# Optimization experiments

Measured on AMD Instinct MI355X. Metric: run time of the kernel, lower is better.

The kernel has to match this reference:

```python
import jax, jax.numpy as jnp
import numpy as np

NUM_HEADS = 16
HEAD_SIZE = 64
D_MODEL = NUM_HEADS * HEAD_SIZE  # 1024


def setup_inputs() -> dict:
    key = jax.random.key(0)
    ks = jax.random.split(key, 12)
    B, S = 4, 2048
    q = jax.random.normal(ks[0], (B, S, D_MODEL), dtype=jnp.float32)
    k = jax.random.normal(ks[1], (B, S, D_MODEL), dtype=jnp.float32)
    v = jax.random.normal(ks[2], (B, S, D_MODEL), dtype=jnp.float32)
    w = jax.random.uniform(ks[3], (B, S), dtype=jnp.float32)
    scale = 1.0 / np.sqrt(D_MODEL)
    Wq = jax.random.normal(ks[4], (D_MODEL, D_MODEL), dtype=jnp.float32) * scale
    Wk = jax.random.normal(ks[5], (D_MODEL, D_MODEL), dtype=jnp.float32) * scale
    Wv = jax.random.normal(ks[6], (D_MODEL, D_MODEL), dtype=jnp.float32) * scale
    Wo = jax.random.normal(ks[7], (D_MODEL, D_MODEL), dtype=jnp.float32) * scale
    bq = jnp.zeros((D_MODEL,), jnp.float32)
    bk = jnp.zeros((D_MODEL,), jnp.float32)
    bv = jnp.zeros((D_MODEL,), jnp.float32)
    bo = jnp.zeros((D_MODEL,), jnp.float32)
    return {"q": q, "k": k, "v": v, "w": w,
            "Wq": Wq, "bq": bq, "Wk": Wk, "bk": bk,
            "Wv": Wv, "bv": bv, "Wo": Wo, "bo": bo}


def reference(q, k, v, w, Wq, bq, Wk, bk, Wv, bv, Wo, bo):
    B, S, _ = q.shape
    H, Dh = NUM_HEADS, HEAD_SIZE

    def split_heads(x):  # [B,S,D] -> [B,H,S,Dh]
        return x.reshape(B, -1, H, Dh).transpose(0, 2, 1, 3)

    q_h = split_heads(q @ Wq + bq)
    k_h = split_heads(k @ Wk + bk)
    v_h = split_heads(v @ Wv + bv)

    # [B,H,Sq,Sk]
    score = jnp.einsum('bhqd,bhkd->bhqk', q_h, k_h) / jnp.sqrt(
        jnp.asarray(Dh, jnp.float32))
    # weighted unnormalized softmax: exp(score)*w / sum (no max subtraction,
    # faithful to original)
    exp_score = jnp.exp(score) * w[:, None, None, :]
    attn = exp_score / (jnp.sum(exp_score, axis=-1, keepdims=True) + 1e-12)

    context = jnp.einsum('bhqk,bhkd->bhqd', attn, v_h)  # [B,H,S,Dh]
    context = context.transpose(0, 2, 1, 3).reshape(B, -1, H * Dh)
    return context @ Wo + bo
```

## Files before the change

### kernel.cpp

```cpp
#include <hip/hip_runtime.h>
#include <hip/hip_bf16.h>

typedef __bf16 bf16x8 __attribute__((ext_vector_type(8)));
typedef float f32x4 __attribute__((ext_vector_type(4)));
typedef float f32x16 __attribute__((ext_vector_type(16)));
typedef unsigned short u16;
typedef unsigned int u32;

#define SB 4
#define SS 2048
#define SD 1024
#define SH 16
#define SDH 64

__device__ __forceinline__ u16 f2bf(float f) {
  union { float f; u32 u; } x; x.f = f;
  u32 r = (x.u + 0x7FFFu + ((x.u >> 16) & 1u)) >> 16;
  return (u16)r;
}

__device__ __forceinline__ void gl_lds16(const void* g, void* l) {
  __builtin_amdgcn_global_load_lds(
      (__attribute__((address_space(1))) void*)g,
      (__attribute__((address_space(3))) void*)l, 16, 0, 0);
}

__global__ void cast_bf16_kernel(const float* __restrict__ in,
                                 u32* __restrict__ out, int n8) {
  int i = blockIdx.x * blockDim.x + threadIdx.x;
  if (i >= n8) return;
  const float4* inp = (const float4*)in;
  float4 a = inp[2 * i], b = inp[2 * i + 1];
  uint4 o;
  asm("v_cvt_pk_bf16_f32 %0, %1, %2" : "=v"(o.x) : "v"(a.x), "v"(a.y));
  asm("v_cvt_pk_bf16_f32 %0, %1, %2" : "=v"(o.y) : "v"(a.z), "v"(a.w));
  asm("v_cvt_pk_bf16_f32 %0, %1, %2" : "=v"(o.z) : "v"(b.x), "v"(b.y));
  asm("v_cvt_pk_bf16_f32 %0, %1, %2" : "=v"(o.w) : "v"(b.z), "v"(b.w));
  ((uint4*)out)[i] = o;
}

__global__ void log2w_kernel(const float* __restrict__ w,
                             float* __restrict__ lwg) {
  int i = blockIdx.x * 256 + threadIdx.x;
  lwg[i] = __builtin_amdgcn_logf(w[i]);
}

__global__ void transpose_cast_kernel(const float* __restrict__ W0,
                                      const float* __restrict__ W1,
                                      const float* __restrict__ W2,
                                      const float* __restrict__ W3,
                                      u16* __restrict__ T0,
                                      u16* __restrict__ T1,
                                      u16* __restrict__ T2,
                                      u16* __restrict__ T3) {
  __shared__ float t[32][33];
  int z = blockIdx.z;
  const float* W = (z == 0) ? W0 : (z == 1) ? W1 : (z == 2) ? W2 : W3;
  u16* Wt = (z == 0) ? T0 : (z == 1) ? T1 : (z == 2) ? T2 : T3;
  int bx = blockIdx.x, by = blockIdx.y;
  int tx = threadIdx.x, ty = threadIdx.y;
#pragma unroll
  for (int j = 0; j < 32; j += 8)
    t[ty + j][tx] = W[(size_t)(by * 32 + ty + j) * SD + bx * 32 + tx];
  __syncthreads();
#pragma unroll
  for (int j = 0; j < 32; j += 8)
    Wt[(size_t)(bx * 32 + ty + j) * SD + by * 32 + tx] = f2bf(t[tx][ty + j]);
}

template <int MODE>
__global__ __launch_bounds__(256, 2)
void gemm_bt(const u16* __restrict__ A, const u16* __restrict__ Bt,
             const float* __restrict__ bias, void* __restrict__ Out,
             int M, int N, int K) {
  __shared__ u16 Asl[2][128 * 64];
  __shared__ u16 Bsl[2][128 * 64];
  const int ntile = N >> 7;
  int bid = blockIdx.x;
  bid = (bid & 7) * ((int)gridDim.x >> 3) + (bid >> 3);
  int m0 = (bid / ntile) * 128, n0 = (bid % ntile) * 128;
  int tid = threadIdx.x;
  int lane = tid & 63, wv = tid >> 6;
  int wr = wv >> 1, wc = wv & 1;

  auto stage = [&](int buf, int k0) {
#pragma unroll
    for (int it = 0; it < 4; ++it) {
      int c = tid + it * 256;
      int row = c >> 3, sl = c & 7;
      int ssl = sl ^ (row & 7);
      gl_lds16(A + (size_t)(m0 + row) * K + k0 + ssl * 8,
               (char*)&Asl[buf][0] + c * 16);
      gl_lds16(Bt + (size_t)(n0 + row) * K + k0 + ssl * 8,
               (char*)&Bsl[buf][0] + c * 16);
    }
  };

  f32x4 acc[4][4] = {};
  stage(0, 0);

  int nk = K >> 6;
  for (int kt = 0; kt < nk; ++kt) {
    int buf = kt & 1;
    if (kt + 1 < nk) {
      stage(buf ^ 1, (kt + 1) << 6);
      asm volatile("s_waitcnt vmcnt(8) lgkmcnt(0)" ::: "memory");
    } else {
      asm volatile("s_waitcnt vmcnt(0) lgkmcnt(0)" ::: "memory");
    }
    __builtin_amdgcn_s_barrier();
#pragma unroll
    for (int kk = 0; kk < 2; ++kk) {
      bf16x8 af[4], bfr[4];
#pragma unroll
      for (int i = 0; i < 4; ++i) {
        int ar = wr * 64 + i * 16 + (lane & 15);
        int abyt = (ar * 128 + (kk * 32 + (lane >> 4) * 8) * 2) ^
                   ((ar & 7) << 4);
        af[i] = *(const bf16x8*)((const char*)&Asl[buf][0] + abyt);
        int br = wc * 64 + i * 16 + (lane & 15);
        int bbyt = (br * 128 + (kk * 32 + (lane >> 4) * 8) * 2) ^
                   ((br & 7) << 4);
        bfr[i] = *(const bf16x8*)((const char*)&Bsl[buf][0] + bbyt);
      }
#pragma unroll
      for (int i = 0; i < 4; ++i)
#pragma unroll
        for (int j = 0; j < 4; ++j)
          acc[i][j] = __builtin_amdgcn_mfma_f32_16x16x32_bf16(
              af[i], bfr[j], acc[i][j], 0, 0, 0);
    }
    __builtin_amdgcn_s_barrier();
  }

  int cg = lane >> 4, cc = lane & 15;
#pragma unroll
  for (int i = 0; i < 4; ++i) {
#pragma unroll
    for (int j = 0; j < 4; ++j) {
#pragma unroll
      for (int r = 0; r < 4; ++r) {
        int m = m0 + wr * 64 + i * 16 + cg * 4 + r;
        int n = n0 + wc * 64 + j * 16 + cc;
        float val = acc[i][j][r];
        if (MODE == 0) {
          val = (val + bias[n]) * 0.18033688011112042f;
          int b = m >> 11, s = m & 2047, h = n >> 6, dh = n & 63;
          ((u16*)Out)[((size_t)((b * SH + h) * SS + s) << 6) + dh] = f2bf(val);
        } else if (MODE == 1) {
          val += bias[n];
          int b = m >> 11, s = m & 2047, h = n >> 6, dh = n & 63;
          size_t off = ((size_t)(b * SH + h) << 17) + ((size_t)(s >> 5) << 11) +
                       ((size_t)(dh >> 4) << 9) +
                       ((size_t)((s & 31) | ((dh & 8) << 2)) << 3) + (dh & 7);
          ((u16*)Out)[off] = f2bf(val);
        } else if (MODE == 2) {
          val += bias[m];
          int h = m >> 6, dh = m & 63, b = n >> 11, s = n & 2047;
          size_t off = ((size_t)(b * SH + h) << 17) + ((size_t)(s >> 4) << 10) +
                       ((size_t)(dh >> 5) << 9) +
                       ((size_t)(((s >> 3) & 1) * 32 + (dh & 31)) << 3) +
                       (s & 7);
          ((u16*)Out)[off] = f2bf(val);
        } else {
          val += bias[n];
          ((float*)Out)[(size_t)m * N + n] = val;
        }
      }
    }
  }
}

__global__ __launch_bounds__(256, 2)
void attn_kernel(const u16* __restrict__ Qh, const u16* __restrict__ Kf,
                 const u16* __restrict__ Vf, const float* __restrict__ lwg,
                 u16* __restrict__ Ctx) {
  __shared__ u16 Kl[4][4096];
  __shared__ u16 Vl[4][4096];

  int bid = blockIdx.x;
  int swz = (bid & 7) * 64 + (bid >> 3);
  int bh = swz >> 3;
  int qt = swz & 7;
  int b = bh >> 4, hh = bh & 15;
  int q0 = qt * 256;
  int tid = threadIdx.x, lane = tid & 63, wv = tid >> 6;
  int ql = lane & 31, h = lane >> 5;
  const size_t basebh = (size_t)bh * (SS * SDH);
  const char* Ksrc = (const char*)(Kf + basebh);
  const char* Vsrc = (const char*)(Vf + basebh);
  const float* lwp = lwg + b * SS;

  bf16x8 qf[2][4];
#pragma unroll
  for (int u = 0; u < 2; ++u) {
    const u16* qp =
        Qh + basebh + (size_t)(q0 + wv * 64 + u * 32 + ql) * SDH + h * 8;
#pragma unroll
    for (int st = 0; st < 4; ++st) qf[u][st] = *(const bf16x8*)(qp + st * 16);
  }

  auto stage = [&](int s, int t) {
#pragma unroll
    for (int it = 0; it < 2; ++it) {
      int c = tid + it * 256;
      gl_lds16(Ksrc + (size_t)t * 8192 + c * 16, (char*)&Kl[s][0] + c * 16);
      gl_lds16(Vsrc + (size_t)t * 8192 + c * 16, (char*)&Vl[s][0] + c * 16);
    }
  };

  f32x16 ctx[2][2] = {};
  float rs[2] = {0.f, 0.f};
  u32 pkA[2][8][2], pkB[2][8][2];

  auto qk = [&](int t, u32 (&pk)[2][8][2]) {
    const char* Ks = (const char*)&Kl[t & 3][0];
    int kvb = t * 64;
#pragma unroll
    for (int kt = 0; kt < 2; ++kt) {
      bf16x8 kf[4];
#pragma unroll
      for (int st = 0; st < 4; ++st)
        kf[st] = *(const bf16x8*)(Ks + (kt * 4 + st) * 1024 + lane * 16);
      float4 lw[4];
#pragma unroll
      for (int e2 = 0; e2 < 4; ++e2)
        lw[e2] = *(const float4*)(lwp + kvb + kt * 32 + e2 * 8 + h * 4);
#pragma unroll
      for (int u = 0; u < 2; ++u) {
        f32x16 sc;
#pragma unroll
        for (int e2 = 0; e2 < 4; ++e2) {
          sc[e2 * 4 + 0] = lw[e2].x;
          sc[e2 * 4 + 1] = lw[e2].y;
          sc[e2 * 4 + 2] = lw[e2].z;
          sc[e2 * 4 + 3] = lw[e2].w;
        }
        __builtin_amdgcn_s_setprio(1);
#pragma unroll
        for (int st = 0; st < 4; ++st)
          sc = __builtin_amdgcn_mfma_f32_32x32x16_bf16(kf[st], qf[u][st], sc,
                                                       0, 0, 0);
        __builtin_amdgcn_s_setprio(0);
#pragma unroll
        for (int e2 = 0; e2 < 4; ++e2) {
          float v0 = __builtin_amdgcn_exp2f(sc[e2 * 4 + 0]);
          float v1 = __builtin_amdgcn_exp2f(sc[e2 * 4 + 1]);
          float v2 = __builtin_amdgcn_exp2f(sc[e2 * 4 + 2]);
          float v3 = __builtin_amdgcn_exp2f(sc[e2 * 4 + 3]);
          rs[u] += (v0 + v1) + (v2 + v3);
          u32 p0, p1;
          asm("v_cvt_pk_bf16_f32 %0, %1, %2" : "=v"(p0) : "v"(v0), "v"(v1));
          asm("v_cvt_pk_bf16_f32 %0, %1, %2" : "=v"(p1) : "v"(v2), "v"(v3));
          pk[u][kt * 4 + e2][0] = p0;
          pk[u][kt * 4 + e2][1] = p1;
        }
      }
    }
  };

  auto pv = [&](int t, u32 (&pk)[2][8][2]) {
    const char* Vs = (const char*)&Vl[t & 3][0];
#pragma unroll
    for (int ksl = 0; ksl < 4; ++ksl) {
      bf16x8 vf0 = *(const bf16x8*)(Vs + (ksl * 2 + 0) * 1024 + lane * 16);
      bf16x8 vf1 = *(const bf16x8*)(Vs + (ksl * 2 + 1) * 1024 + lane * 16);
#pragma unroll
      for (int u = 0; u < 2; ++u) {
        u32 d0 = pk[u][2 * ksl][0], d1 = pk[u][2 * ksl][1];
        u32 s0 = pk[u][2 * ksl + 1][0], s1 = pk[u][2 * ksl + 1][1];
        asm("v_permlane32_swap_b32 %0, %1" : "+v"(d0), "+v"(s0));
        asm("v_permlane32_swap_b32 %0, %1" : "+v"(d1), "+v"(s1));
        union { u32 uu[4]; bf16x8 v; } pa;
        pa.uu[0] = d0; pa.uu[1] = d1; pa.uu[2] = s0; pa.uu[3] = s1;
        __builtin_amdgcn_s_setprio(1);
        ctx[u][0] = __builtin_amdgcn_mfma_f32_32x32x16_bf16(pa.v, vf0,
                                                            ctx[u][0], 0, 0, 0);
        ctx[u][1] = __builtin_amdgcn_mfma_f32_32x32x16_bf16(pa.v, vf1,
                                                            ctx[u][1], 0, 0, 0);
        __builtin_amdgcn_s_setprio(0);
      }
    }
  };

  stage(0, 0);
  stage(1, 1);

  asm volatile("s_waitcnt vmcnt(4)" ::: "memory");
  __builtin_amdgcn_s_barrier();
  stage(2, 2);
  qk(0, pkA);

  for (int t = 1; t < 30; t += 2) {
    asm volatile("s_waitcnt vmcnt(4)" ::: "memory");
    __builtin_amdgcn_s_barrier();
    stage((t + 2) & 3, t + 2);
    pv(t - 1, pkA);
    qk(t, pkB);

    asm volatile("s_waitcnt vmcnt(4)" ::: "memory");
    __builtin_amdgcn_s_barrier();
    if (t + 3 < 32) stage((t + 3) & 3, t + 3);
    pv(t, pkB);
    qk(t + 1, pkA);
  }

  asm volatile("s_waitcnt vmcnt(0)" ::: "memory");
  __builtin_amdgcn_s_barrier();
  pv(30, pkA);
  qk(31, pkB);
  pv(31, pkB);

#pragma unroll
  for (int u = 0; u < 2; ++u) {
    float rsu = rs[u];
    rsu += __shfl_xor(rsu, 32, 64);
    float rinv = 1.0f / (rsu + 1e-12f);
#pragma unroll
    for (int reg = 0; reg < 16; ++reg) {
      int qrow = (reg & 3) + 8 * (reg >> 2) + 4 * h;
      float ri = __shfl(rinv, qrow, 64);
      int srow = q0 + wv * 64 + u * 32 + qrow;
      size_t base = ((size_t)(b * SS + srow) << 10) + hh * SDH;
      Ctx[base + ql] = f2bf(ctx[u][0][reg] * ri);
      Ctx[base + 32 + ql] = f2bf(ctx[u][1][reg] * ri);
    }
  }
}

extern "C" void kernel_launch(void* const* d_in, const int* in_sizes, int n_in,
                              void* d_out, int out_size, void* d_ws,
                              size_t ws_size, hipStream_t stream) {
  const float* q = (const float*)d_in[0];
  const float* k = (const float*)d_in[1];
  const float* v = (const float*)d_in[2];
  const float* w = (const float*)d_in[3];
  const float* Wq = (const float*)d_in[4];
  const float* bq = (const float*)d_in[5];
  const float* Wk = (const float*)d_in[6];
  const float* bk = (const float*)d_in[7];
  const float* Wv = (const float*)d_in[8];
  const float* bv = (const float*)d_in[9];
  const float* Wo = (const float*)d_in[10];
  const float* bo = (const float*)d_in[11];
  float* out = (float*)d_out;

  char* ws = (char*)d_ws;
  const size_t SZ = (size_t)8192 * 1024 * 2;
  u16* qb = (u16*)(ws);
  u16* kb = (u16*)(ws + SZ);
  u16* vb = (u16*)(ws + 2 * SZ);
  u16* WqT = (u16*)(ws + 3 * SZ);
  u16* WkT = WqT + 1024 * 1024;
  u16* WvT = WkT + 1024 * 1024;
  u16* WoT = WvT + 1024 * 1024;
  u16* Qh = (u16*)(ws + 3 * SZ + (size_t)4 * 1024 * 1024 * 2);
  u16* Kf = Qh + (size_t)8192 * 1024;
  u16* Vf = Kf + (size_t)8192 * 1024;
  float* lwg = (float*)(ws + 3 * SZ + (size_t)4 * 1024 * 1024 * 2 +
                        (size_t)3 * 8192 * 1024 * 2);
  u16* Ctx = qb;

  cast_bf16_kernel<<<4096, 256, 0, stream>>>(q, (u32*)qb, 1048576);
  cast_bf16_kernel<<<4096, 256, 0, stream>>>(k, (u32*)kb, 1048576);
  cast_bf16_kernel<<<4096, 256, 0, stream>>>(v, (u32*)vb, 1048576);
  log2w_kernel<<<32, 256, 0, stream>>>(w, lwg);
  dim3 tb(32, 8), tg(32, 32, 4);
  transpose_cast_kernel<<<tg, tb, 0, stream>>>(Wq, Wk, Wv, Wo,
                                               WqT, WkT, WvT, WoT);

  gemm_bt<0><<<512, 256, 0, stream>>>(qb, WqT, bq, Qh, 8192, 1024, 1024);
  gemm_bt<1><<<512, 256, 0, stream>>>(kb, WkT, bk, Kf, 8192, 1024, 1024);
  gemm_bt<2><<<512, 256, 0, stream>>>(WvT, vb, bv, Vf, 1024, 8192, 1024);

  attn_kernel<<<512, 256, 0, stream>>>(Qh, Kf, Vf, lwg, Ctx);

  gemm_bt<3><<<512, 256, 0, stream>>>(Ctx, WoT, bo, out, 8192, 1024, 1024);
}
```

Baseline: 210.2 us.

## Split attention KV sequence across two wave groups with LDS reduction

The attention block grows to 512 threads. Each of the two halves of 4 waves processes half the KV tiles (a split-K over keys) using its own double-buffered LDS region, and the partial context and row sums are then reduced through shared memory before normalization and store. The QK and PV phases are merged into one per-tile compute step, and the pipeline changes from a 4-stage software-pipelined ping-pong to a simpler 2-stage wait-all loop. The aim is more waves per CU to hide latency, at the cost of a less overlapped pipeline, 64KB of LDS per block, and extra reduction barriers.

```diff
diff --git a/kernel.cpp b/kernel.cpp
--- a/kernel.cpp
+++ b/kernel.cpp
@@ -3,6 +3,7 @@
 
 typedef __bf16 bf16x8 __attribute__((ext_vector_type(8)));
 typedef float f32x4 __attribute__((ext_vector_type(4)));
+typedef float f32x8 __attribute__((ext_vector_type(8)));
 typedef float f32x16 __attribute__((ext_vector_type(16)));
 typedef unsigned short u16;
 typedef unsigned int u32;
@@ -171,12 +172,11 @@
   }
 }
 
-__global__ __launch_bounds__(256, 2)
+__global__ __launch_bounds__(512, 4)
 void attn_kernel(const u16* __restrict__ Qh, const u16* __restrict__ Kf,
                  const u16* __restrict__ Vf, const float* __restrict__ lwg,
                  u16* __restrict__ Ctx) {
-  __shared__ u16 Kl[4][4096];
-  __shared__ u16 Vl[4][4096];
+  __shared__ __align__(16) char smem[65536];
 
   int bid = blockIdx.x;
   int swz = (bid & 7) * 64 + (bid >> 3);
@@ -185,60 +185,65 @@
   int b = bh >> 4, hh = bh & 15;
   int q0 = qt * 256;
   int tid = threadIdx.x, lane = tid & 63, wv = tid >> 6;
+  int qw = wv & 3, kvh = wv >> 2;
   int ql = lane & 31, h = lane >> 5;
+  int tl = tid & 255;
   const size_t basebh = (size_t)bh * (SS * SDH);
   const char* Ksrc = (const char*)(Kf + basebh);
   const char* Vsrc = (const char*)(Vf + basebh);
   const float* lwp = lwg + b * SS;
+  char* mybase = smem + kvh * 32768;
 
   bf16x8 qf[2][4];
 #pragma unroll
   for (int u = 0; u < 2; ++u) {
     const u16* qp =
-        Qh + basebh + (size_t)(q0 + wv * 64 + u * 32 + ql) * SDH + h * 8;
+        Qh + basebh + (size_t)(q0 + qw * 64 + u * 32 + ql) * SDH + h * 8;
 #pragma unroll
     for (int st = 0; st < 4; ++st) qf[u][st] = *(const bf16x8*)(qp + st * 16);
   }
 
-  auto stage = [&](int s, int t) {
+  auto stage = [&](int s, int th) {
+    char* dst = mybase + s * 16384;
 #pragma unroll
     for (int it = 0; it < 2; ++it) {
-      int c = tid + it * 256;
-      gl_lds16(Ksrc + (size_t)t * 8192 + c * 16, (char*)&Kl[s][0] + c * 16);
-      gl_lds16(Vsrc + (size_t)t * 8192 + c * 16, (char*)&Vl[s][0] + c * 16);
+      int c = tl + it * 256;
+      gl_lds16(Ksrc + (size_t)th * 8192 + c * 16, dst + c * 16);
+      gl_lds16(Vsrc + (size_t)th * 8192 + c * 16, dst + 8192 + c * 16);
     }
   };
 
   f32x16 ctx[2][2] = {};
   float rs[2] = {0.f, 0.f};
-  u32 pkA[2][8][2], pkB[2][8][2];
-
-  auto qk = [&](int t, u32 (&pk)[2][8][2]) {
-    const char* Ks = (const char*)&Kl[t & 3][0];
-    int kvb = t * 64;
+
+  auto compute = [&](int s, int th) {
+    const char* Ks = mybase + s * 16384;
+    const char* Vs = Ks + 8192;
+    int kvb = th * 64;
+    u32 pk[2][8][2];
 #pragma unroll
     for (int kt = 0; kt < 2; ++kt) {
       bf16x8 kf[4];
 #pragma unroll
       for (int st = 0; st < 4; ++st)
         kf[st] = *(const bf16x8*)(Ks + (kt * 4 + st) * 1024 + lane * 16);
-      float4 lw[4];
-#pragma unroll
-      for (int e2 = 0; e2 < 4; ++e2)
-        lw[e2] = *(const float4*)(lwp + kvb + kt * 32 + e2 * 8 + h * 4);
+      const float* lb = lwp + kvb + kt * 32 + h * 4;
+      f32x4 l0 = *(const f32x4*)(lb);
+      f32x4 l1 = *(const f32x4*)(lb + 8);
+      f32x4 l2 = *(const f32x4*)(lb + 16);
+      f32x4 l3 = *(const f32x4*)(lb + 24);
+      f32x8 lo = __builtin_shufflevector(l0, l1, 0, 1, 2, 3, 4, 5, 6, 7);
+      f32x8 hi = __builtin_shufflevector(l2, l3, 0, 1, 2, 3, 4, 5, 6, 7);
+      f32x16 lwv = __builtin_shufflevector(lo, hi, 0, 1, 2, 3, 4, 5, 6, 7, 8,
+                                           9, 10, 11, 12, 13, 14, 15);
 #pragma unroll
       for (int u = 0; u < 2; ++u) {
-        f32x16 sc;
-#pragma unroll
-        for (int e2 = 0; e2 < 4; ++e2) {
-          sc[e2 * 4 + 0] = lw[e2].x;
-          sc[e2 * 4 + 1] = lw[e2].y;
-          sc[e2 * 4 + 2] = lw[e2].z;
-          sc[e2 * 4 + 3] = lw[e2].w;
-        }
         __builtin_amdgcn_s_setprio(1);
-#pragma unroll
-        for (int st = 0; st < 4; ++st)
+        f32x16 sc =
+            __builtin_amdgcn_mfma_f32_32x32x16_bf16(kf[0], qf[u][0], lwv,
+                                                    0, 0, 0);
+#pragma unroll
+        for (int st = 1; st < 4; ++st)
           sc = __builtin_amdgcn_mfma_f32_32x32x16_bf16(kf[st], qf[u][st], sc,
                                                        0, 0, 0);
         __builtin_amdgcn_s_setprio(0);
@@ -257,10 +262,6 @@
         }
       }
     }
-  };
-
-  auto pv = [&](int t, u32 (&pk)[2][8][2]) {
-    const char* Vs = (const char*)&Vl[t & 3][0];
 #pragma unroll
     for (int ksl = 0; ksl < 4; ++ksl) {
       bf16x8 vf0 = *(const bf16x8*)(Vs + (ksl * 2 + 0) * 1024 + lane * 16);
@@ -283,47 +284,82 @@
     }
   };
 
-  stage(0, 0);
-  stage(1, 1);
-
-  asm volatile("s_waitcnt vmcnt(4)" ::: "memory");
-  __builtin_amdgcn_s_barrier();
-  stage(2, 2);
-  qk(0, pkA);
-
-  for (int t = 1; t < 30; t += 2) {
-    asm volatile("s_waitcnt vmcnt(4)" ::: "memory");
+  const int t0 = kvh * 16;
+  stage(0, t0);
+
+  for (int i = 0; i < 16; ++i) {
+    asm volatile("s_waitcnt vmcnt(0)" ::: "memory");
     __builtin_amdgcn_s_barrier();
-    stage((t + 2) & 3, t + 2);
-    pv(t - 1, pkA);
-    qk(t, pkB);
-
-    asm volatile("s_waitcnt vmcnt(4)" ::: "memory");
-    __builtin_amdgcn_s_barrier();
-    if (t + 3 < 32) stage((t + 3) & 3, t + 3);
-    pv(t, pkB);
-    qk(t + 1, pkA);
-  }
-
-  asm volatile("s_waitcnt vmcnt(0)" ::: "memory");
-  __builtin_amdgcn_s_barrier();
-  pv(30, pkA);
-  qk(31, pkB);
-  pv(31, pkB);
-
+    if (i + 1 < 16) stage((i + 1) & 1, t0 + i + 1);
+    compute(i & 1, t0 + i);
+  }
+
+  float rsu[2];
 #pragma unroll
   for (int u = 0; u < 2; ++u) {
-    float rsu = rs[u];
-    rsu += __shfl_xor(rsu, 32, 64);
-    float rinv = 1.0f / (rsu + 1e-12f);
-#pragma unroll
-    for (int reg = 0; reg < 16; ++reg) {
-      int qrow = (reg & 3) + 8 * (reg >> 2) + 4 * h;
-      float ri = __shfl(rinv, qrow, 64);
-      int srow = q0 + wv * 64 + u * 32 + qrow;
-      size_t base = ((size_t)(b * SS + srow) << 10) + hh * SDH;
-      Ctx[base + ql] = f2bf(ctx[u][0][reg] * ri);
-      Ctx[base + 32 + ql] = f2bf(ctx[u][1][reg] * ri);
+    float r = rs[u];
+    r += __shfl_xor(r, 32, 64);
+    rsu[u] = r;
+  }
+
+  float* rsbuf = (float*)smem;
+  float* cbuf = (float*)(smem + 4096);
+
+  __syncthreads();
+  rsbuf[((kvh * 4 + qw) * 2 + 0) * 32 + ql] = rsu[0];
+  rsbuf[((kvh * 4 + qw) * 2 + 1) * 32 + ql] = rsu[1];
+  if (kvh == 1) {
+#pragma unroll
+    for (int j = 0; j < 2; ++j)
+#pragma unroll
+      for (int reg = 0; reg < 16; ++reg)
+        cbuf[((qw * 2 + j) * 16 + reg) * 64 + lane] = ctx[0][j][reg];
+  }
+  __syncthreads();
+
+  float rinv[2];
+#pragma unroll
+  for (int u = 0; u < 2; ++u) {
+    float rtot = rsbuf[((0 * 4 + qw) * 2 + u) * 32 + ql] +
+                 rsbuf[((1 * 4 + qw) * 2 + u) * 32 + ql];
+    rinv[u] = 1.0f / (rtot + 1e-12f);
+  }
+
+  if (kvh == 0) {
+#pragma unroll
+    for (int j = 0; j < 2; ++j)
+#pragma unroll
+      for (int reg = 0; reg < 16; ++reg)
+        ctx[0][j][reg] += cbuf[((qw * 2 + j) * 16 + reg) * 64 + lane];
+  }
+  __syncthreads();
+  if (kvh == 1) {
+#pragma unroll
+    for (int j = 0; j < 2; ++j)
+#pragma unroll
+      for (int reg = 0; reg < 16; ++reg)
+        cbuf[((qw * 2 + j) * 16 + reg) * 64 + lane] = ctx[1][j][reg];
+  }
+  __syncthreads();
+
+  if (kvh == 0) {
+#pragma unroll
+    for (int u = 0; u < 2; ++u) {
+#pragma unroll
+      for (int reg = 0; reg < 16; ++reg) {
+        int qrow = (reg & 3) + 8 * (reg >> 2) + 4 * h;
+        float ri = __shfl(rinv[u], qrow, 64);
+        int srow = q0 + qw * 64 + u * 32 + qrow;
+        size_t base = ((size_t)(b * SS + srow) << 10) + hh * SDH;
+        float c0 = ctx[u][0][reg];
+        float c1 = ctx[u][1][reg];
+        if (u == 1) {
+          c0 += cbuf[((qw * 2 + 0) * 16 + reg) * 64 + lane];
+          c1 += cbuf[((qw * 2 + 1) * 16 + reg) * 64 + lane];
+        }
+        Ctx[base + ql] = f2bf(c0 * ri);
+        Ctx[base + 32 + ql] = f2bf(c1 * ri);
+      }
     }
   }
 }
@@ -373,7 +409,7 @@
   gemm_bt<1><<<512, 256, 0, stream>>>(kb, WkT, bk, Kf, 8192, 1024, 1024);
   gemm_bt<2><<<512, 256, 0, stream>>>(WvT, vb, bv, Vf, 1024, 8192, 1024);
 
-  attn_kernel<<<512, 256, 0, stream>>>(Qh, Kf, Vf, lwg, Ctx);
+  attn_kernel<<<512, 512, 0, stream>>>(Qh, Kf, Vf, lwg, Ctx);
 
   gemm_bt<3><<<512, 256, 0, stream>>>(Ctx, WoT, bo, out, 8192, 1024, 1024);
 }
```

Measured after the change: 575.3 us. 174% more time.

## Shrink attention tiles to 128 queries and double-buffer with higher occupancy

Applied to the files above, without the earlier changes.

The attention kernel now gives each block 128 query rows instead of 256, with each wave handling 32 rows. This doubles the grid to 1024 blocks and raises launch bounds to 4 blocks per CU. The 4-stage K/V ring with software-pipelined QK/PV across tiles is replaced by a simple 2-stage double buffer with a full vmcnt(0) wait each iteration. The aim is more parallelism and lower register and LDS pressure, at the cost of twice as much K/V loading per query and less intra-wave latency hiding.

```diff
diff --git a/kernel.cpp b/kernel.cpp
--- a/kernel.cpp
+++ b/kernel.cpp
@@ -3,6 +3,7 @@
 
 typedef __bf16 bf16x8 __attribute__((ext_vector_type(8)));
 typedef float f32x4 __attribute__((ext_vector_type(4)));
+typedef float f32x8 __attribute__((ext_vector_type(8)));
 typedef float f32x16 __attribute__((ext_vector_type(16)));
 typedef unsigned short u16;
 typedef unsigned int u32;
@@ -171,160 +172,119 @@
   }
 }
 
-__global__ __launch_bounds__(256, 2)
+__global__ __launch_bounds__(256, 4)
 void attn_kernel(const u16* __restrict__ Qh, const u16* __restrict__ Kf,
                  const u16* __restrict__ Vf, const float* __restrict__ lwg,
                  u16* __restrict__ Ctx) {
-  __shared__ u16 Kl[4][4096];
-  __shared__ u16 Vl[4][4096];
+  __shared__ __align__(16) char smem[2][16384];
 
   int bid = blockIdx.x;
-  int swz = (bid & 7) * 64 + (bid >> 3);
-  int bh = swz >> 3;
-  int qt = swz & 7;
+  int swz = (bid & 7) * 128 + (bid >> 3);
+  int bh = swz >> 4;
+  int qt = swz & 15;
   int b = bh >> 4, hh = bh & 15;
-  int q0 = qt * 256;
-  int tid = threadIdx.x, lane = tid & 63, wv = tid >> 6;
+  int q0 = qt * 128;
+  int tid = threadIdx.x, lane = tid & 63, qw = tid >> 6;
   int ql = lane & 31, h = lane >> 5;
   const size_t basebh = (size_t)bh * (SS * SDH);
   const char* Ksrc = (const char*)(Kf + basebh);
   const char* Vsrc = (const char*)(Vf + basebh);
   const float* lwp = lwg + b * SS;
 
-  bf16x8 qf[2][4];
-#pragma unroll
-  for (int u = 0; u < 2; ++u) {
-    const u16* qp =
-        Qh + basebh + (size_t)(q0 + wv * 64 + u * 32 + ql) * SDH + h * 8;
-#pragma unroll
-    for (int st = 0; st < 4; ++st) qf[u][st] = *(const bf16x8*)(qp + st * 16);
+  bf16x8 qf[4];
+  {
+    const u16* qp = Qh + basebh + (size_t)(q0 + qw * 32 + ql) * SDH + h * 8;
+#pragma unroll
+    for (int st = 0; st < 4; ++st) qf[st] = *(const bf16x8*)(qp + st * 16);
   }
 
   auto stage = [&](int s, int t) {
-#pragma unroll
-    for (int it = 0; it < 2; ++it) {
+    char* dst = &smem[s][0];
+#pragma unroll
+    for (int it = 0; it < 4; ++it) {
       int c = tid + it * 256;
-      gl_lds16(Ksrc + (size_t)t * 8192 + c * 16, (char*)&Kl[s][0] + c * 16);
-      gl_lds16(Vsrc + (size_t)t * 8192 + c * 16, (char*)&Vl[s][0] + c * 16);
+      gl_lds16((c < 512 ? Ksrc : Vsrc - 8192) + (size_t)t * 8192 + c * 16,
+               dst + c * 16);
     }
   };
 
-  f32x16 ctx[2][2] = {};
-  float rs[2] = {0.f, 0.f};
-  u32 pkA[2][8][2], pkB[2][8][2];
-
-  auto qk = [&](int t, u32 (&pk)[2][8][2]) {
-    const char* Ks = (const char*)&Kl[t & 3][0];
+  f32x16 ctx0 = {}, ctx1 = {};
+  float rs = 0.f;
+
+  stage(0, 0);
+
+  for (int t = 0; t < 32; ++t) {
+    int s = t & 1;
+    asm volatile("s_waitcnt vmcnt(0)" ::: "memory");
+    __builtin_amdgcn_s_barrier();
+    if (t + 1 < 32) stage(s ^ 1, t + 1);
+
+    const char* Ks = &smem[s][0];
+    const char* Vs = Ks + 8192;
     int kvb = t * 64;
+    u32 pk[8][2];
 #pragma unroll
     for (int kt = 0; kt < 2; ++kt) {
       bf16x8 kf[4];
 #pragma unroll
       for (int st = 0; st < 4; ++st)
         kf[st] = *(const bf16x8*)(Ks + (kt * 4 + st) * 1024 + lane * 16);
-      float4 lw[4];
-#pragma unroll
-      for (int e2 = 0; e2 < 4; ++e2)
-        lw[e2] = *(const float4*)(lwp + kvb + kt * 32 + e2 * 8 + h * 4);
-#pragma unroll
-      for (int u = 0; u < 2; ++u) {
-        f32x16 sc;
-#pragma unroll
-        for (int e2 = 0; e2 < 4; ++e2) {
-          sc[e2 * 4 + 0] = lw[e2].x;
-          sc[e2 * 4 + 1] = lw[e2].y;
-          sc[e2 * 4 + 2] = lw[e2].z;
-          sc[e2 * 4 + 3] = lw[e2].w;
-        }
-        __builtin_amdgcn_s_setprio(1);
-#pragma unroll
-        for (int st = 0; st < 4; ++st)
-          sc = __builtin_amdgcn_mfma_f32_32x32x16_bf16(kf[st], qf[u][st], sc,
-                                                       0, 0, 0);
-        __builtin_amdgcn_s_setprio(0);
-#pragma unroll
-        for (int e2 = 0; e2 < 4; ++e2) {
-          float v0 = __builtin_amdgcn_exp2f(sc[e2 * 4 + 0]);
-          float v1 = __builtin_amdgcn_exp2f(sc[e2 * 4 + 1]);
-          float v2 = __builtin_amdgcn_exp2f(sc[e2 * 4 + 2]);
-          float v3 = __builtin_amdgcn_exp2f(sc[e2 * 4 + 3]);
-          rs[u] += (v0 + v1) + (v2 + v3);
-          u32 p0, p1;
-          asm("v_cvt_pk_bf16_f32 %0, %1, %2" : "=v"(p0) : "v"(v0), "v"(v1));
-          asm("v_cvt_pk_bf16_f32 %0, %1, %2" : "=v"(p1) : "v"(v2), "v"(v3));
-          pk[u][kt * 4 + e2][0] = p0;
-          pk[u][kt * 4 + e2][1] = p1;
-        }
+      const float* lb = lwp + kvb + kt * 32 + h * 4;
+      f32x4 l0 = *(const f32x4*)(lb);
+      f32x4 l1 = *(const f32x4*)(lb + 8);
+      f32x4 l2 = *(const f32x4*)(lb + 16);
+      f32x4 l3 = *(const f32x4*)(lb + 24);
+      f32x8 lo = __builtin_shufflevector(l0, l1, 0, 1, 2, 3, 4, 5, 6, 7);
+      f32x8 hi = __builtin_shufflevector(l2, l3, 0, 1, 2, 3, 4, 5, 6, 7);
+      f32x16 sc = __builtin_shufflevector(lo, hi, 0, 1, 2, 3, 4, 5, 6, 7, 8,
+                                          9, 10, 11, 12, 13, 14, 15);
+      __builtin_amdgcn_s_setprio(1);
+#pragma unroll
+      for (int st = 0; st < 4; ++st)
+        sc = __builtin_amdgcn_mfma_f32_32x32x16_bf16(kf[st], qf[st], sc,
+                                                     0, 0, 0);
+      __builtin_amdgcn_s_setprio(0);
+#pragma unroll
+      for (int e2 = 0; e2 < 4; ++e2) {
+        float v0 = __builtin_amdgcn_exp2f(sc[e2 * 4 + 0]);
+        float v1 = __builtin_amdgcn_exp2f(sc[e2 * 4 + 1]);
+        float v2 = __builtin_amdgcn_exp2f(sc[e2 * 4 + 2]);
+        float v3 = __builtin_amdgcn_exp2f(sc[e2 * 4 + 3]);
+        rs += (v0 + v1) + (v2 + v3);
+        u32 p0, p1;
+        asm("v_cvt_pk_bf16_f32 %0, %1, %2" : "=v"(p0) : "v"(v0), "v"(v1));
+        asm("v_cvt_pk_bf16_f32 %0, %1, %2" : "=v"(p1) : "v"(v2), "v"(v3));
+        pk[kt * 4 + e2][0] = p0;
+        pk[kt * 4 + e2][1] = p1;
       }
     }
-  };
-
-  auto pv = [&](int t, u32 (&pk)[2][8][2]) {
-    const char* Vs = (const char*)&Vl[t & 3][0];
 #pragma unroll
     for (int ksl = 0; ksl < 4; ++ksl) {
       bf16x8 vf0 = *(const bf16x8*)(Vs + (ksl * 2 + 0) * 1024 + lane * 16);
       bf16x8 vf1 = *(const bf16x8*)(Vs + (ksl * 2 + 1) * 1024 + lane * 16);
-#pragma unroll
-      for (int u = 0; u < 2; ++u) {
-        u32 d0 = pk[u][2 * ksl][0], d1 = pk[u][2 * ksl][1];
-        u32 s0 = pk[u][2 * ksl + 1][0], s1 = pk[u][2 * ksl + 1][1];
-        asm("v_permlane32_swap_b32 %0, %1" : "+v"(d0), "+v"(s0));
-        asm("v_permlane32_swap_b32 %0, %1" : "+v"(d1), "+v"(s1));
-        union { u32 uu[4]; bf16x8 v; } pa;
-        pa.uu[0] = d0; pa.uu[1] = d1; pa.uu[2] = s0; pa.uu[3] = s1;
-        __builtin_amdgcn_s_setprio(1);
-        ctx[u][0] = __builtin_amdgcn_mfma_f32_32x32x16_bf16(pa.v, vf0,
-                                                            ctx[u][0], 0, 0, 0);
-        ctx[u][1] = __builtin_amdgcn_mfma_f32_32x32x16_bf16(pa.v, vf1,
-                                                            ctx[u][1], 0, 0, 0);
-        __builtin_amdgcn_s_setprio(0);
-      }
-    }
-  };
-
-  stage(0, 0);
-  stage(1, 1);
-
-  asm volatile("s_waitcnt vmcnt(4)" ::: "memory");
-  __builtin_amdgcn_s_barrier();
-  stage(2, 2);
-  qk(0, pkA);
-
-  for (int t = 1; t < 30; t += 2) {
-    asm volatile("s_waitcnt vmcnt(4)" ::: "memory");
-    __builtin_amdgcn_s_barrier();
-    stage((t + 2) & 3, t + 2);
-    pv(t - 1, pkA);
-    qk(t, pkB);
-
-    asm volatile("s_waitcnt vmcnt(4)" ::: "memory");
-    __builtin_amdgcn_s_barrier();
-    if (t + 3 < 32) stage((t + 3) & 3, t + 3);
-    pv(t, pkB);
-    qk(t + 1, pkA);
-  }
-
-  asm volatile("s_waitcnt vmcnt(0)" ::: "memory");
-  __builtin_amdgcn_s_barrier();
-  pv(30, pkA);
-  qk(31, pkB);
-  pv(31, pkB);
-
-#pragma unroll
-  for (int u = 0; u < 2; ++u) {
-    float rsu = rs[u];
-    rsu += __shfl_xor(rsu, 32, 64);
-    float rinv = 1.0f / (rsu + 1e-12f);
-#pragma unroll
-    for (int reg = 0; reg < 16; ++reg) {
-      int qrow = (reg & 3) + 8 * (reg >> 2) + 4 * h;
-      float ri = __shfl(rinv, qrow, 64);
-      int srow = q0 + wv * 64 + u * 32 + qrow;
-      size_t base = ((size_t)(b * SS + srow) << 10) + hh * SDH;
-      Ctx[base + ql] = f2bf(ctx[u][0][reg] * ri);
-      Ctx[base + 32 + ql] = f2bf(ctx[u][1][reg] * ri);
-    }
+      u32 d0 = pk[2 * ksl][0], d1 = pk[2 * ksl][1];
+      u32 s0 = pk[2 * ksl + 1][0], s1 = pk[2 * ksl + 1][1];
+      asm("v_permlane32_swap_b32 %0, %1" : "+v"(d0), "+v"(s0));
+      asm("v_permlane32_swap_b32 %0, %1" : "+v"(d1), "+v"(s1));
+      union { u32 uu[4]; bf16x8 v; } pa;
+      pa.uu[0] = d0; pa.uu[1] = d1; pa.uu[2] = s0; pa.uu[3] = s1;
+      __builtin_amdgcn_s_setprio(1);
+      ctx0 = __builtin_amdgcn_mfma_f32_32x32x16_bf16(pa.v, vf0, ctx0, 0, 0, 0);
+      ctx1 = __builtin_amdgcn_mfma_f32_32x32x16_bf16(pa.v, vf1, ctx1, 0, 0, 0);
+      __builtin_amdgcn_s_setprio(0);
+    }
+  }
+
+  rs += __shfl_xor(rs, 32, 64);
+  float rinv = 1.0f / (rs + 1e-12f);
+#pragma unroll
+  for (int reg = 0; reg < 16; ++reg) {
+    int qrow = (reg & 3) + 8 * (reg >> 2) + 4 * h;
+    float ri = __shfl(rinv, qrow, 64);
+    int srow = q0 + qw * 32 + qrow;
+    size_t base = ((size_t)(b * SS + srow) << 10) + hh * SDH;
+    Ctx[base + ql] = f2bf(ctx0[reg] * ri);
+    Ctx[base + 32 + ql] = f2bf(ctx1[reg] * ri);
   }
 }
 
@@ -373,7 +333,7 @@
   gemm_bt<1><<<512, 256, 0, stream>>>(kb, WkT, bk, Kf, 8192, 1024, 1024);
   gemm_bt<2><<<512, 256, 0, stream>>>(WvT, vb, bv, Vf, 1024, 8192, 1024);
 
-  attn_kernel<<<512, 256, 0, stream>>>(Qh, Kf, Vf, lwg, Ctx);
+  attn_kernel<<<1024, 256, 0, stream>>>(Qh, Kf, Vf, lwg, Ctx);
 
   gemm_bt<3><<<512, 256, 0, stream>>>(Ctx, WoT, bo, out, 8192, 1024, 1024);
 }
```

New measurement: 222.4 us. 5.8% more time.

## Restructure attention pipeline with split K/V staging and LDS log-weights; merge casts

Applied to the files above, without the earlier changes.

The attention main loop is rewritten to stage K and V tiles separately, with per-tile waits, and to run a simple per-tile qk-then-pv sequence. This replaces the earlier software-pipelined loop that interleaved pv(t-1) with qk(t) across two probability register sets. The per-batch log2 weights are copied into LDS once per block and fed directly as the MFMA accumulator initialiser, instead of being read from global memory on every tile. The three q/k/v cast launches are merged into one 2D-grid launch to cut launch overhead. Dropping the double-buffered probability registers lowers register pressure, but it gives up overlap between the exp work and the PV MFMAs, and the extra 8KB of LDS may reduce occupancy.

```diff
diff --git a/kernel.cpp b/kernel.cpp
--- a/kernel.cpp
+++ b/kernel.cpp
@@ -3,6 +3,7 @@
 
 typedef __bf16 bf16x8 __attribute__((ext_vector_type(8)));
 typedef float f32x4 __attribute__((ext_vector_type(4)));
+typedef float f32x8 __attribute__((ext_vector_type(8)));
 typedef float f32x16 __attribute__((ext_vector_type(16)));
 typedef unsigned short u16;
 typedef unsigned int u32;
@@ -25,10 +26,15 @@
       (__attribute__((address_space(3))) void*)l, 16, 0, 0);
 }
 
-__global__ void cast_bf16_kernel(const float* __restrict__ in,
-                                 u32* __restrict__ out, int n8) {
-  int i = blockIdx.x * blockDim.x + threadIdx.x;
-  if (i >= n8) return;
+__global__ void cast3_kernel(const float* __restrict__ q,
+                             const float* __restrict__ k,
+                             const float* __restrict__ v,
+                             u32* __restrict__ oq, u32* __restrict__ ok,
+                             u32* __restrict__ ov) {
+  int sel = blockIdx.y;
+  const float* in = (sel == 0) ? q : (sel == 1) ? k : v;
+  u32* out = (sel == 0) ? oq : (sel == 1) ? ok : ov;
+  int i = blockIdx.x * 256 + threadIdx.x;
   const float4* inp = (const float4*)in;
   float4 a = inp[2 * i], b = inp[2 * i + 1];
   uint4 o;
@@ -177,6 +183,7 @@
                  u16* __restrict__ Ctx) {
   __shared__ u16 Kl[4][4096];
   __shared__ u16 Vl[4][4096];
+  __shared__ float lwl[SS];
 
   int bid = blockIdx.x;
   int swz = (bid & 7) * 64 + (bid >> 3);
@@ -189,7 +196,14 @@
   const size_t basebh = (size_t)bh * (SS * SDH);
   const char* Ksrc = (const char*)(Kf + basebh);
   const char* Vsrc = (const char*)(Vf + basebh);
-  const float* lwp = lwg + b * SS;
+
+  {
+    const float4* src = (const float4*)(lwg + b * SS);
+    float4 r0 = src[tid];
+    float4 r1 = src[tid + 256];
+    ((float4*)lwl)[tid] = r0;
+    ((float4*)lwl)[tid + 256] = r1;
+  }
 
   bf16x8 qf[2][4];
 #pragma unroll
@@ -200,20 +214,24 @@
     for (int st = 0; st < 4; ++st) qf[u][st] = *(const bf16x8*)(qp + st * 16);
   }
 
-  auto stage = [&](int s, int t) {
-#pragma unroll
-    for (int it = 0; it < 2; ++it) {
-      int c = tid + it * 256;
-      gl_lds16(Ksrc + (size_t)t * 8192 + c * 16, (char*)&Kl[s][0] + c * 16);
-      gl_lds16(Vsrc + (size_t)t * 8192 + c * 16, (char*)&Vl[s][0] + c * 16);
-    }
+  __syncthreads();
+
+  auto stageK = [&](int s, int t) {
+    const char* p = Ksrc + (size_t)t * 8192;
+    gl_lds16(p + tid * 16, (char*)&Kl[s][0] + tid * 16);
+    gl_lds16(p + 4096 + tid * 16, (char*)&Kl[s][0] + 4096 + tid * 16);
+  };
+  auto stageV = [&](int s, int t) {
+    const char* p = Vsrc + (size_t)t * 8192;
+    gl_lds16(p + tid * 16, (char*)&Vl[s][0] + tid * 16);
+    gl_lds16(p + 4096 + tid * 16, (char*)&Vl[s][0] + 4096 + tid * 16);
   };
 
   f32x16 ctx[2][2] = {};
   float rs[2] = {0.f, 0.f};
-  u32 pkA[2][8][2], pkB[2][8][2];
-
-  auto qk = [&](int t, u32 (&pk)[2][8][2]) {
+  u32 pk[2][8][2];
+
+  auto qk = [&](int t) {
     const char* Ks = (const char*)&Kl[t & 3][0];
     int kvb = t * 64;
 #pragma unroll
@@ -222,23 +240,22 @@
 #pragma unroll
       for (int st = 0; st < 4; ++st)
         kf[st] = *(const bf16x8*)(Ks + (kt * 4 + st) * 1024 + lane * 16);
-      float4 lw[4];
-#pragma unroll
-      for (int e2 = 0; e2 < 4; ++e2)
-        lw[e2] = *(const float4*)(lwp + kvb + kt * 32 + e2 * 8 + h * 4);
+      const float* lb = lwl + kvb + kt * 32 + h * 4;
+      f32x4 l0 = *(const f32x4*)(lb);
+      f32x4 l1 = *(const f32x4*)(lb + 8);
+      f32x4 l2 = *(const f32x4*)(lb + 16);
+      f32x4 l3 = *(const f32x4*)(lb + 24);
+      f32x8 lo = __builtin_shufflevector(l0, l1, 0, 1, 2, 3, 4, 5, 6, 7);
+      f32x8 hi = __builtin_shufflevector(l2, l3, 0, 1, 2, 3, 4, 5, 6, 7);
+      f32x16 lwv = __builtin_shufflevector(lo, hi, 0, 1, 2, 3, 4, 5, 6, 7, 8,
+                                           9, 10, 11, 12, 13, 14, 15);
 #pragma unroll
       for (int u = 0; u < 2; ++u) {
-        f32x16 sc;
-#pragma unroll
-        for (int e2 = 0; e2 < 4; ++e2) {
-          sc[e2 * 4 + 0] = lw[e2].x;
-          sc[e2 * 4 + 1] = lw[e2].y;
-          sc[e2 * 4 + 2] = lw[e2].z;
-          sc[e2 * 4 + 3] = lw[e2].w;
-        }
         __builtin_amdgcn_s_setprio(1);
-#pragma unroll
-        for (int st = 0; st < 4; ++st)
+        f32x16 sc = __builtin_amdgcn_mfma_f32_32x32x16_bf16(
+            kf[0], qf[u][0], lwv, 0, 0, 0);
+#pragma unroll
+        for (int st = 1; st < 4; ++st)
           sc = __builtin_amdgcn_mfma_f32_32x32x16_bf16(kf[st], qf[u][st], sc,
                                                        0, 0, 0);
         __builtin_amdgcn_s_setprio(0);
@@ -259,7 +276,7 @@
     }
   };
 
-  auto pv = [&](int t, u32 (&pk)[2][8][2]) {
+  auto pv = [&](int t) {
     const char* Vs = (const char*)&Vl[t & 3][0];
 #pragma unroll
     for (int ksl = 0; ksl < 4; ++ksl) {
@@ -283,33 +300,30 @@
     }
   };
 
-  stage(0, 0);
-  stage(1, 1);
-
+  stageK(0, 0);
+  stageV(0, 0);
+  stageK(1, 1);
+  stageV(1, 1);
+
+  for (int t = 0; t < 30; ++t) {
+    asm volatile("s_waitcnt vmcnt(6)" ::: "memory");
+    __builtin_amdgcn_s_barrier();
+    stageK((t + 2) & 3, t + 2);
+    qk(t);
+    asm volatile("s_waitcnt vmcnt(6)" ::: "memory");
+    stageV((t + 2) & 3, t + 2);
+    pv(t);
+  }
+  asm volatile("s_waitcnt vmcnt(6)" ::: "memory");
+  __builtin_amdgcn_s_barrier();
+  qk(30);
   asm volatile("s_waitcnt vmcnt(4)" ::: "memory");
+  pv(30);
+  asm volatile("s_waitcnt vmcnt(2)" ::: "memory");
   __builtin_amdgcn_s_barrier();
-  stage(2, 2);
-  qk(0, pkA);
-
-  for (int t = 1; t < 30; t += 2) {
-    asm volatile("s_waitcnt vmcnt(4)" ::: "memory");
-    __builtin_amdgcn_s_barrier();
-    stage((t + 2) & 3, t + 2);
-    pv(t - 1, pkA);
-    qk(t, pkB);
-
-    asm volatile("s_waitcnt vmcnt(4)" ::: "memory");
-    __builtin_amdgcn_s_barrier();
-    if (t + 3 < 32) stage((t + 3) & 3, t + 3);
-    pv(t, pkB);
-    qk(t + 1, pkA);
-  }
-
+  qk(31);
   asm volatile("s_waitcnt vmcnt(0)" ::: "memory");
-  __builtin_amdgcn_s_barrier();
-  pv(30, pkA);
-  qk(31, pkB);
-  pv(31, pkB);
+  pv(31);
 
 #pragma unroll
   for (int u = 0; u < 2; ++u) {
@@ -361,9 +375,8 @@
                         (size_t)3 * 8192 * 1024 * 2);
   u16* Ctx = qb;
 
-  cast_bf16_kernel<<<4096, 256, 0, stream>>>(q, (u32*)qb, 1048576);
-  cast_bf16_kernel<<<4096, 256, 0, stream>>>(k, (u32*)kb, 1048576);
-  cast_bf16_kernel<<<4096, 256, 0, stream>>>(v, (u32*)vb, 1048576);
+  cast3_kernel<<<dim3(4096, 3), 256, 0, stream>>>(q, k, v, (u32*)qb,
+                                                  (u32*)kb, (u32*)vb);
   log2w_kernel<<<32, 256, 0, stream>>>(w, lwg);
   dim3 tb(32, 8), tg(32, 32, 4);
   transpose_cast_kernel<<<tg, tb, 0, stream>>>(Wq, Wk, Wv, Wo,
```

Result: no change. 212.6 us (+1.2%).
